# Kernel optimization log

Measured on AMD Instinct MI355X. Metric: run time of the kernel, lower is better.

Reference implementation:

```python
import jax, jax.numpy as jnp
import numpy as np
from jax import lax

B = 8; IMG = 224; P = 16; D = 192; DEPTH = 8
H = IMG // P; W = H; L = H * W
D_IN = 384; D_STATE = 16; D_CONV = 4; DT_R = 12; NCLS = 1000
EPS = 1e-5


def _ln(x, w, b):
    m = x.mean(-1, keepdims=True)
    v = ((x - m) ** 2).mean(-1, keepdims=True)
    return (x - m) * lax.rsqrt(v + EPS) * w + b


def _mixer(seq, p):
    # seq: (B, L, D) -> Mamba selective-scan mixer
    xz = jnp.einsum('bld,ed->ble', seq, p['in_proj_w'])  # (B,L,2*D_IN)
    u, z = jnp.split(xz, 2, axis=-1)
    # causal depthwise conv1d over L
    uc = lax.conv_general_dilated(u.transpose(0, 2, 1), p['conv_w'][:, None, :], (1,),
                                  [(D_CONV - 1, 0)], feature_group_count=D_IN,
                                  dimension_numbers=('NCH', 'OIH', 'NCH'))
    u = jax.nn.silu(uc.transpose(0, 2, 1) + p['conv_b'])
    xdbl = jnp.einsum('bld,ed->ble', u, p['x_proj_w'])  # (B,L,DT_R+2*D_STATE)
    dt = xdbl[..., :DT_R]
    Bm = xdbl[..., DT_R:DT_R + D_STATE]
    Cm = xdbl[..., DT_R + D_STATE:]
    delta = jax.nn.softplus(jnp.einsum('blr,dr->bld', dt, p['dt_w']) + p['dt_b'])
    A = -jnp.exp(p['A_log'])  # (D_IN, D_STATE)

    def step(h, inp):
        d_t, B_t, C_t, u_t = inp  # (b,D_IN),(b,N),(b,N),(b,D_IN)
        h = h * jnp.exp(d_t[..., None] * A) + (d_t * u_t)[..., None] * B_t[:, None, :]
        return h, jnp.einsum('bdn,bn->bd', h, C_t)

    h0 = jnp.zeros((seq.shape[0], D_IN, D_STATE), seq.dtype)
    _, ys = lax.scan(step, h0, (delta.transpose(1, 0, 2), Bm.transpose(1, 0, 2),
                                Cm.transpose(1, 0, 2), u.transpose(1, 0, 2)))
    y = ys.transpose(1, 0, 2) + u * p['D']
    y = y * jax.nn.silu(z)
    return jnp.einsum('bld,cd->blc', y, p['out_proj_w'])


def _stack(seq, params):
    # Block: residual = residual + hidden; hidden = mixer(LN(residual))
    def body(carry, p):
        hidden, residual = carry
        residual = residual + hidden
        hidden = _mixer(_ln(residual, p['ln_w'], p['ln_b']), p)
        return (hidden, residual), None

    (hidden, residual), _ = lax.scan(body, (seq, jnp.zeros_like(seq)), params)
    return hidden + residual


def _forward(x, patch_w, patch_b, pe_ln_w, pe_ln_b, ln_w, ln_b, in_proj_w, conv_w,
             conv_b, x_proj_w, dt_w, dt_b, A_log, Dp, out_proj_w, out_norm_w,
             out_norm_b, head_ln_w, head_ln_b, head_w, head_b):
    b = x.shape[0]
    # patch embed: conv(stride=patch) + LayerNorm over channels
    feat = lax.conv_general_dilated(x, patch_w, (P, P), 'VALID',
                                    dimension_numbers=('NCHW', 'OIHW', 'NCHW'))
    feat = feat + patch_b[None, :, None, None]  # (B, D, H, W)
    feat = _ln(feat.transpose(0, 2, 3, 1), pe_ln_w, pe_ln_b).transpose(0, 3, 1, 2)
    # CrossScan: 4 directional unrollings
    x0 = feat.reshape(b, D, L)
    x1 = feat.transpose(0, 1, 3, 2).reshape(b, D, L)
    xs = jnp.stack([x0, x1, x0[..., ::-1], x1[..., ::-1]], axis=1)  # (B,4,D,L)
    dirs = xs.transpose(1, 0, 3, 2)  # (4,B,L,D)
    params = {'ln_w': ln_w, 'ln_b': ln_b, 'in_proj_w': in_proj_w, 'conv_w': conv_w,
              'conv_b': conv_b, 'x_proj_w': x_proj_w, 'dt_w': dt_w, 'dt_b': dt_b,
              'A_log': A_log, 'D': Dp, 'out_proj_w': out_proj_w}
    outs = jax.vmap(_stack)(dirs, params)  # (4,B,L,D)
    # CrossMerge
    ys = outs.transpose(1, 0, 3, 2)  # (B,4,D,L)
    ym = ys[:, 0:2] + ys[:, 2:4][..., ::-1]
    y = ym[:, 0] + ym[:, 1].reshape(b, D, W, H).transpose(0, 1, 3, 2).reshape(b, D, L)
    y = _ln(y.transpose(0, 2, 1), out_norm_w, out_norm_b)  # (B,L,D)
    y = _ln(y.reshape(b, H, W, D), head_ln_w, head_ln_b)
    return y.mean(axis=(1, 2)) @ head_w.T + head_b  # (B, NCLS)


def setup_inputs() -> dict:
    key = jax.random.key(0)
    ks = jax.random.split(key, 10)
    rn = lambda k, s, sc=0.02: jax.random.normal(k, s, jnp.float32) * sc
    A_init = jnp.broadcast_to(jnp.arange(1, D_STATE + 1, dtype=jnp.float32),
                              (4, DEPTH, D_IN, D_STATE))
    return {
        'x': jax.random.normal(ks[0], (B, 3, IMG, IMG), jnp.float32),
        'patch_w': rn(ks[1], (D, 3, P, P)),
        'patch_b': jnp.zeros((D,), jnp.float32),
        'pe_ln_w': jnp.ones((D,), jnp.float32),
        'pe_ln_b': jnp.zeros((D,), jnp.float32),
        'ln_w': jnp.ones((4, DEPTH, D), jnp.float32),
        'ln_b': jnp.zeros((4, DEPTH, D), jnp.float32),
        'in_proj_w': rn(ks[2], (4, DEPTH, 2 * D_IN, D)),
        'conv_w': rn(ks[3], (4, DEPTH, D_IN, D_CONV), 0.1),
        'conv_b': jnp.zeros((4, DEPTH, D_IN), jnp.float32),
        'x_proj_w': rn(ks[4], (4, DEPTH, DT_R + 2 * D_STATE, D_IN)),
        'dt_w': rn(ks[5], (4, DEPTH, D_IN, DT_R), 0.1),
        'dt_b': jnp.log(jnp.expm1(0.01)) + rn(ks[6], (4, DEPTH, D_IN), 0.02),
        'A_log': jnp.log(A_init),
        'Dp': jnp.ones((4, DEPTH, D_IN), jnp.float32),
        'out_proj_w': rn(ks[7], (4, DEPTH, D, D_IN)),
        'out_norm_w': jnp.ones((D,), jnp.float32),
        'out_norm_b': jnp.zeros((D,), jnp.float32),
        'head_ln_w': jnp.ones((D,), jnp.float32),
        'head_ln_b': jnp.zeros((D,), jnp.float32),
        'head_w': rn(ks[8], (NCLS, D)),
        'head_b': jnp.zeros((NCLS,), jnp.float32),
    }


def reference(x, patch_w, patch_b, pe_ln_w, pe_ln_b, ln_w, ln_b, in_proj_w, conv_w,
              conv_b, x_proj_w, dt_w, dt_b, A_log, Dp, out_proj_w, out_norm_w,
              out_norm_b, head_ln_w, head_ln_b, head_w, head_b):
    return _forward(x, patch_w, patch_b, pe_ln_w, pe_ln_b, ln_w, ln_b, in_proj_w,
                    conv_w, conv_b, x_proj_w, dt_w, dt_b, A_log, Dp, out_proj_w,
                    out_norm_w, out_norm_b, head_ln_w, head_ln_b, head_w, head_b)
```

## Files before the change

### kernel.cpp

```cpp
#include <hip/hip_runtime.h>

#define B_ 8
#define IMGSZ 224
#define PATCH 16
#define D_ 192
#define DEPTH_ 8
#define H_ 14
#define W_ 14
#define L_ 196
#define DIN 384
#define DSTATE 16
#define DCONV 4
#define DTR 12
#define NCLS_ 1000
#define EPS_ 1e-5f
#define ROWS_PER_DIR (B_*L_)
#define M_TOTAL (4*ROWS_PER_DIR)

typedef unsigned short ushort_t;
typedef unsigned int uint_t;
typedef __attribute__((ext_vector_type(8)))  short bf16x8;
typedef __attribute__((ext_vector_type(16))) float f32x16;

__device__ __forceinline__ ushort_t f2bf(float f) {
  uint_t u = __builtin_bit_cast(uint_t, f);
  u += 0x7fffu + ((u >> 16) & 1u);
  return (ushort_t)(u >> 16);
}

__global__ __launch_bounds__(256) void k_cvt3(
    const float* __restrict__ s0, const float* __restrict__ s1,
    const float* __restrict__ s2, ushort_t* __restrict__ dst)
{
  int i = blockIdx.x*256 + threadIdx.x;
  if (i >= 1806336) return;
  const float* src;
  int off;
  if (i < 36864)        { src = s0; off = i; }
  else if (i < 1216512) { src = s1; off = i - 36864; }
  else                  { src = s2; off = i - 1216512; }
  float4 v = reinterpret_cast<const float4*>(src)[off];
  ushort4 o;
  o.x = f2bf(v.x); o.y = f2bf(v.y); o.z = f2bf(v.z); o.w = f2bf(v.w);
  reinterpret_cast<ushort4*>(dst)[i] = o;
}

__global__ __launch_bounds__(256) void k_cvt_xw(const float* __restrict__ src,
                                                ushort_t* __restrict__ dst)
{
  int idx = blockIdx.x*256 + threadIdx.x;
  if (idx >= 32*64*384) return;
  int g = idx / (64*384);
  int r = (idx / 384) % 64;
  int k = idx % 384;
  float v = (r < 44) ? src[((size_t)g*44 + r)*384 + k] : 0.f;
  dst[idx] = f2bf(v);
}

__global__ __launch_bounds__(256) void k_im2col(const float* __restrict__ x,
                                                ushort_t* __restrict__ Xp)
{
  int idx = blockIdx.x*256 + threadIdx.x;
  if (idx >= ROWS_PER_DIR*768) return;
  int row = idx / 768, k = idx - row*768;
  int b = row / L_, l = row - b*L_;
  int hh = l / W_, ww = l - hh*W_;
  int c = k >> 8, rem = k & 255, pi = rem >> 4, pj = rem & 15;
  float v = x[(((size_t)b*3 + c)*IMGSZ + hh*PATCH + pi)*IMGSZ + ww*PATCH + pj];
  Xp[idx] = f2bf(v);
}

template<int KT>
__global__ __launch_bounds__(64) void k_gemm2(
    const ushort_t* __restrict__ X, const ushort_t* __restrict__ W,
    float* __restrict__ C, int N, int nb, int wstride, int rows_per_dir)
{
  int row0 = blockIdx.x*32, col0 = blockIdx.y*64;
  int dir = row0 / rows_per_dir;
  const ushort_t* Wp = W + (size_t)dir*wstride;
  int l = threadIdx.x;
  int r31 = l & 31, khalf = (l >> 5)*8;
  const ushort_t* aptr  = X  + (size_t)(row0 + r31)*KT + khalf;
  const ushort_t* b0ptr = Wp + (size_t)(col0 + r31)*KT + khalf;
  const ushort_t* b1ptr = b0ptr + (size_t)32*KT;
  f32x16 acc00 = {}, acc01 = {}, acc10 = {}, acc11 = {};
  #pragma unroll
  for (int k = 0; k < KT; k += 32) {
    bf16x8 a0 = *reinterpret_cast<const bf16x8*>(aptr + k);
    bf16x8 a1 = *reinterpret_cast<const bf16x8*>(aptr + k + 16);
    bf16x8 b00 = *reinterpret_cast<const bf16x8*>(b0ptr + k);
    bf16x8 b01 = *reinterpret_cast<const bf16x8*>(b0ptr + k + 16);
    bf16x8 b10 = *reinterpret_cast<const bf16x8*>(b1ptr + k);
    bf16x8 b11 = *reinterpret_cast<const bf16x8*>(b1ptr + k + 16);
    acc00 = __builtin_amdgcn_mfma_f32_32x32x16_bf16(a0, b00, acc00, 0, 0, 0);
    acc01 = __builtin_amdgcn_mfma_f32_32x32x16_bf16(a1, b01, acc01, 0, 0, 0);
    acc10 = __builtin_amdgcn_mfma_f32_32x32x16_bf16(a0, b10, acc10, 0, 0, 0);
    acc11 = __builtin_amdgcn_mfma_f32_32x32x16_bf16(a1, b11, acc11, 0, 0, 0);
  }
  int c0 = col0 + r31, c1 = col0 + 32 + r31;
  #pragma unroll
  for (int r = 0; r < 16; ++r) {
    int row = (r & 3) + 8*(r >> 2) + 4*(l >> 5);
    float* crow = C + (size_t)(row0 + row)*N;
    if (c0 < nb) crow[c0] = acc00[r] + acc01[r];
    if (c1 < nb) crow[c1] = acc10[r] + acc11[r];
  }
}

__global__ __launch_bounds__(64) void k_peln(
    const float* __restrict__ Cp, const float* __restrict__ pb,
    const float* __restrict__ plw, const float* __restrict__ plb,
    const float* __restrict__ lnw, const float* __restrict__ lnb,
    float* __restrict__ residual, ushort_t* __restrict__ xln)
{
  int blk = blockIdx.x;
  int b = blk / L_, l = blk - b*L_;
  int hh = l / W_, ww = l - hh*W_;
  int lane = threadIdx.x;
  float v[3]; float s = 0.f;
  #pragma unroll
  for (int i = 0; i < 3; ++i) {
    int d = lane + i*64;
    float t = Cp[(size_t)blk*D_ + d] + pb[d];
    v[i] = t; s += t;
  }
  #pragma unroll
  for (int off = 32; off; off >>= 1) s += __shfl_xor(s, off);
  float m = s*(1.f/D_); float q = 0.f;
  #pragma unroll
  for (int i = 0; i < 3; ++i) { float dd = v[i]-m; q += dd*dd; }
  #pragma unroll
  for (int off = 32; off; off >>= 1) q += __shfl_xor(q, off);
  float inv = rsqrtf(q*(1.f/D_)+EPS_);
  float nv[3]; s = 0.f;
  #pragma unroll
  for (int i = 0; i < 3; ++i) {
    int d = lane + i*64;
    nv[i] = (v[i]-m)*inv*plw[d] + plb[d];
    s += nv[i];
  }
  #pragma unroll
  for (int off = 32; off; off >>= 1) s += __shfl_xor(s, off);
  float m2 = s*(1.f/D_); q = 0.f;
  #pragma unroll
  for (int i = 0; i < 3; ++i) { float dd = nv[i]-m2; q += dd*dd; }
  #pragma unroll
  for (int off = 32; off; off >>= 1) q += __shfl_xor(q, off);
  float inv2 = rsqrtf(q*(1.f/D_)+EPS_);
  int l1 = ww*W_ + hh;
  size_t rr[4];
  rr[0] = ((size_t)(0*B_+b))*L_ + l;
  rr[1] = ((size_t)(1*B_+b))*L_ + l1;
  rr[2] = ((size_t)(2*B_+b))*L_ + (L_-1-l);
  rr[3] = ((size_t)(3*B_+b))*L_ + (L_-1-l1);
  #pragma unroll
  for (int i = 0; i < 3; ++i) {
    int d = lane + i*64;
    float nrm = (nv[i]-m2)*inv2;
    #pragma unroll
    for (int k = 0; k < 4; ++k) {
      residual[rr[k]*D_+d] = nv[i];
      xln[rr[k]*D_+d] = f2bf(nrm*lnw[(size_t)(k*DEPTH_)*D_+d] + lnb[(size_t)(k*DEPTH_)*D_+d]);
    }
  }
}

__global__ __launch_bounds__(256) void k_conv(
    const float* __restrict__ xz, const float* __restrict__ cw, const float* __restrict__ cb,
    float* __restrict__ u, ushort_t* __restrict__ ub, int layer)
{
  int idx = blockIdx.x*256 + threadIdx.x;
  if (idx >= M_TOTAL*96) return;
  int row = idx / 96, d4 = (idx - row*96)*4;
  int kdir = row / ROWS_PER_DIR;
  int l = row % L_;
  size_t pbase = (size_t)(kdir*DEPTH_+layer)*DIN + d4;
  const float* cwp = cw + pbase*DCONV;
  float wv[16];
  #pragma unroll
  for (int i = 0; i < 4; ++i)
    ((float4*)wv)[i] = ((const float4*)cwp)[i];
  float4 bias = *reinterpret_cast<const float4*>(&cb[pbase]);
  float acc[4] = {bias.x, bias.y, bias.z, bias.w};
  #pragma unroll
  for (int t = 0; t < DCONV; ++t) {
    int ll = l - 3 + t;
    if (ll >= 0) {
      float4 xv = *reinterpret_cast<const float4*>(&xz[((size_t)row + (ll - l))*768 + d4]);
      acc[0] += xv.x * wv[0*4 + t];
      acc[1] += xv.y * wv[1*4 + t];
      acc[2] += xv.z * wv[2*4 + t];
      acc[3] += xv.w * wv[3*4 + t];
    }
  }
  float4 o; ushort4 ob;
  o.x = acc[0] / (1.f + __expf(-acc[0]));
  o.y = acc[1] / (1.f + __expf(-acc[1]));
  o.z = acc[2] / (1.f + __expf(-acc[2]));
  o.w = acc[3] / (1.f + __expf(-acc[3]));
  ob.x = f2bf(o.x); ob.y = f2bf(o.y); ob.z = f2bf(o.z); ob.w = f2bf(o.w);
  *reinterpret_cast<float4*>(&u[(size_t)row*DIN + d4]) = o;
  *reinterpret_cast<ushort4*>(&ub[(size_t)row*DIN + d4]) = ob;
}

#define SCHUNK 14
#define NCHUNK 14
__global__ __launch_bounds__(256, 3) void k_scan(
    const float* __restrict__ u, const float* __restrict__ xdbl,
    const float* __restrict__ xz,
    const float* __restrict__ Alog, const float* __restrict__ Dp,
    const float* __restrict__ dtw, const float* __restrict__ dtb,
    ushort_t* __restrict__ yg, int layer)
{
  int blk = blockIdx.x;
  int kdir = blk / (B_*24);
  int rem = blk % (B_*24);
  int b = rem / 24, dc = rem % 24;
  int tid = threadIdx.x;
  int st = tid & 15, ch = tid >> 4;
  size_t pl = (size_t)(kdir*DEPTH_+layer)*DIN + dc*16 + ch;
  float a = -expf(Alog[pl*DSTATE + st]);
  size_t rowbase = ((size_t)kdir*B_ + b)*L_;

  int ll = tid >> 4, cc = tid & 15;
  bool ldr = tid < 224;
  size_t plc = (size_t)(kdir*DEPTH_+layer)*DIN + dc*16 + cc;
  float Dv3 = Dp[plc];
  float dwt[12]; float dbias = dtb[plc];
  #pragma unroll
  for (int i = 0; i < 3; ++i)
    ((float4*)dwt)[i] = ((const float4*)(dtw + plc*DTR))[i];

  __shared__ __align__(16) float sd[16][20], su[16][20], sB[16][20],
                                 sC[16][20], sz[16][20];
  __shared__ __align__(16) float sp[SCHUNK][16][20];

  float rd=0.f, ru=0.f, rB=0.f, rC=0.f, rz=0.f;
  if (ldr) {
    size_t r = rowbase + ll;
    float xv[12];
    #pragma unroll
    for (int i = 0; i < 3; ++i) ((float4*)xv)[i] = ((const float4*)(xdbl + r*44))[i];
    float acc = dbias;
    #pragma unroll
    for (int t = 0; t < DTR; ++t) acc += xv[t]*dwt[t];
    rd = (acc > 20.f) ? acc : log1pf(__expf(acc));
    ru = u[r*DIN + dc*16 + cc];
    rB = xdbl[r*44 + DTR + cc];
    rC = xdbl[r*44 + DTR + DSTATE + cc];
    rz = xz[r*768 + DIN + dc*16 + cc];
  }

  float h = 0.f;
  for (int chk = 0; chk < NCHUNK; ++chk) {
    if (ldr) { sd[cc][ll]=rd; su[cc][ll]=ru; sB[cc][ll]=rB; sC[cc][ll]=rC; sz[cc][ll]=rz; }
    __syncthreads();
    if (chk+1 < NCHUNK && ldr) {
      size_t r = rowbase + (chk+1)*SCHUNK + ll;
      float xv[12];
      #pragma unroll
      for (int i = 0; i < 3; ++i) ((float4*)xv)[i] = ((const float4*)(xdbl + r*44))[i];
      float acc = dbias;
      #pragma unroll
      for (int t = 0; t < DTR; ++t) acc += xv[t]*dwt[t];
      rd = (acc > 20.f) ? acc : log1pf(__expf(acc));
      ru = u[r*DIN + dc*16 + cc];
      rB = xdbl[r*44 + DTR + cc];
      rC = xdbl[r*44 + DTR + DSTATE + cc];
      rz = xz[r*768 + DIN + dc*16 + cc];
    }
    float dlv[16], ulv[16], Bvv[16], Cvv[16];
    #pragma unroll
    for (int i = 0; i < 4; ++i) {
      ((float4*)dlv)[i] = ((const float4*)&sd[ch][0])[i];
      ((float4*)ulv)[i] = ((const float4*)&su[ch][0])[i];
      ((float4*)Bvv)[i] = ((const float4*)&sB[st][0])[i];
      ((float4*)Cvv)[i] = ((const float4*)&sC[st][0])[i];
    }
    float E[SCHUNK];
    #pragma unroll
    for (int l = 0; l < SCHUNK; ++l) E[l] = __expf(dlv[l]*a);
    #pragma unroll
    for (int l = 0; l < SCHUNK; ++l) {
      h = h*E[l] + dlv[l]*ulv[l]*Bvv[l];
      sp[l][ch][st] = h*Cvv[l];
    }
    __syncthreads();
    if (ldr) {
      float pv[16];
      #pragma unroll
      for (int i = 0; i < 4; ++i)
        ((float4*)pv)[i] = ((const float4*)&sp[ll][cc][0])[i];
      float s = 0.f;
      #pragma unroll
      for (int i = 0; i < 16; ++i) s += pv[i];
      float ul = su[cc][ll];
      float z  = sz[cc][ll];
      float yv = (s + ul*Dv3) * (z / (1.f + __expf(-z)));
      yg[(rowbase + chk*SCHUNK + ll)*DIN + dc*16 + cc] = f2bf(yv);
    }
    __syncthreads();
  }
}

template<int LAST>
__global__ __launch_bounds__(384) void k_outln(
    const ushort_t* __restrict__ X, const ushort_t* __restrict__ W,
    float* __restrict__ residual,
    const float* __restrict__ lnw, const float* __restrict__ lnb,
    ushort_t* __restrict__ xln, int layer)
{
  int row0 = blockIdx.x*32;
  int dir = row0 / ROWS_PER_DIR;
  const ushort_t* Wp = W + (size_t)dir*(DEPTH_*D_*DIN);
  int tid = threadIdx.x;
  int wv = tid >> 6;
  int l  = tid & 63;
  int col0 = wv*32;
  int r31 = l & 31, khalf = (l >> 5)*8;
  const ushort_t* aptr = X  + (size_t)(row0 + r31)*DIN + khalf;
  const ushort_t* bptr = Wp + (size_t)(col0 + r31)*DIN + khalf;
  f32x16 acc0 = {}, acc1 = {};
  #pragma unroll
  for (int k = 0; k < DIN; k += 32) {
    bf16x8 a0 = *reinterpret_cast<const bf16x8*>(aptr + k);
    bf16x8 b0 = *reinterpret_cast<const bf16x8*>(bptr + k);
    bf16x8 a1 = *reinterpret_cast<const bf16x8*>(aptr + k + 16);
    bf16x8 b1 = *reinterpret_cast<const bf16x8*>(bptr + k + 16);
    acc0 = __builtin_amdgcn_mfma_f32_32x32x16_bf16(a0, b0, acc0, 0, 0, 0);
    acc1 = __builtin_amdgcn_mfma_f32_32x32x16_bf16(a1, b1, acc1, 0, 0, 0);
  }
  __shared__ __align__(16) float Cs[32][196];
  __shared__ float sred[32][12], qred[32][12], sm[32], si[32];
  #pragma unroll
  for (int r = 0; r < 16; ++r) {
    int row = (r & 3) + 8*(r >> 2) + 4*(l >> 5);
    Cs[row][col0 + r31] = acc0[r] + acc1[r];
  }
  __syncthreads();
  int rr = tid / 12, jj = tid - rr*12;
  int c0 = jj*16;
  float* resrow = residual + (size_t)(row0+rr)*D_ + c0;
  float v[16];
  float s = 0.f, q = 0.f;
  #pragma unroll
  for (int i = 0; i < 16; i += 4) {
    float4 rv = *reinterpret_cast<const float4*>(resrow + i);
    float4 cv = *reinterpret_cast<const float4*>(&Cs[rr][c0 + i]);
    v[i+0] = rv.x + cv.x; v[i+1] = rv.y + cv.y;
    v[i+2] = rv.z + cv.z; v[i+3] = rv.w + cv.w;
  }
  #pragma unroll
  for (int i = 0; i < 16; ++i) { s += v[i]; q += v[i]*v[i]; }
  #pragma unroll
  for (int i = 0; i < 16; i += 4) {
    float4 o = make_float4(v[i], v[i+1], v[i+2], v[i+3]);
    *reinterpret_cast<float4*>(resrow + i) = o;
  }
  if (!LAST) {
    sred[rr][jj] = s; qred[rr][jj] = q;
    __syncthreads();
    if (tid < 32) {
      float S = 0.f, Q = 0.f;
      #pragma unroll
      for (int j = 0; j < 12; ++j) { S += sred[tid][j]; Q += qred[tid][j]; }
      float m = S*(1.f/D_);
      float var = Q*(1.f/D_) - m*m;
      sm[tid] = m; si[tid] = rsqrtf(var + EPS_);
    }
    __syncthreads();
    float m = sm[rr], inv = si[rr];
    const float* w = lnw + (size_t)(dir*DEPTH_ + layer + 1)*D_ + c0;
    const float* bb = lnb + (size_t)(dir*DEPTH_ + layer + 1)*D_ + c0;
    ushort_t* xrow = xln + (size_t)(row0+rr)*D_ + c0;
    #pragma unroll
    for (int i = 0; i < 16; ++i)
      xrow[i] = f2bf((v[i]-m)*inv*w[i] + bb[i]);
  }
}

__global__ __launch_bounds__(64) void k_combine(
    const float* __restrict__ res,
    const float* __restrict__ onw, const float* __restrict__ onb,
    const float* __restrict__ hlw, const float* __restrict__ hlb,
    float* __restrict__ ynorm)
{
  int blk = blockIdx.x;
  int b = blk / L_, l = blk % L_;
  int hh = l / W_, ww = l % W_;
  int l1 = ww*W_ + hh;
  size_t r0 = ((size_t)(0*B_+b))*L_ + l;
  size_t r1 = ((size_t)(1*B_+b))*L_ + l1;
  size_t r2 = ((size_t)(2*B_+b))*L_ + (L_-1-l);
  size_t r3 = ((size_t)(3*B_+b))*L_ + (L_-1-l1);
  int lane = threadIdx.x;
  float v[3]; float s = 0.f;
  #pragma unroll
  for (int i=0;i<3;i++){
    int d = lane + i*64;
    float t = res[r0*D_+d] + res[r1*D_+d] + res[r2*D_+d] + res[r3*D_+d];
    v[i]=t; s+=t;
  }
  #pragma unroll
  for (int off=32;off;off>>=1) s += __shfl_xor(s,off);
  float m = s*(1.f/D_); float q=0.f;
  #pragma unroll
  for (int i=0;i<3;i++){ float dd=v[i]-m; q+=dd*dd; }
  #pragma unroll
  for (int off=32;off;off>>=1) q += __shfl_xor(q,off);
  float inv = rsqrtf(q*(1.f/D_)+EPS_);
  float v2[3]; s = 0.f;
  #pragma unroll
  for (int i=0;i<3;i++){ int d=lane+i*64; float t=(v[i]-m)*inv*onw[d]+onb[d]; v2[i]=t; s+=t; }
  #pragma unroll
  for (int off=32;off;off>>=1) s += __shfl_xor(s,off);
  float m2 = s*(1.f/D_); q=0.f;
  #pragma unroll
  for (int i=0;i<3;i++){ float dd=v2[i]-m2; q+=dd*dd; }
  #pragma unroll
  for (int off=32;off;off>>=1) q += __shfl_xor(q,off);
  float inv2 = rsqrtf(q*(1.f/D_)+EPS_);
  #pragma unroll
  for (int i=0;i<3;i++){ int d=lane+i*64; ynorm[((size_t)b*L_+l)*D_+d] = (v2[i]-m2)*inv2*hlw[d]+hlb[d]; }
}

__global__ __launch_bounds__(192) void k_mean(const float* __restrict__ ynorm, float* __restrict__ ybar)
{
  int b = blockIdx.x, d = threadIdx.x;
  float s = 0.f;
  for (int l = 0; l < L_; ++l) s += ynorm[((size_t)b*L_+l)*D_ + d];
  ybar[b*D_+d] = s * (1.f/L_);
}

__global__ __launch_bounds__(256) void k_head(
    const float* __restrict__ ybar, const float* __restrict__ hw, const float* __restrict__ hb,
    float* __restrict__ out)
{
  __shared__ float ys[D_];
  int b = blockIdx.x >> 2;
  int c = (blockIdx.x & 3)*256 + threadIdx.x;
  for (int i = threadIdx.x; i < D_; i += 256) ys[i] = ybar[b*D_+i];
  __syncthreads();
  if (c < NCLS_) {
    float acc = hb[c];
    const float* wr = hw + (size_t)c*D_;
    for (int dd = 0; dd < D_; dd += 4) {
      float4 a4 = *reinterpret_cast<const float4*>(&ys[dd]);
      float4 b4 = *reinterpret_cast<const float4*>(&wr[dd]);
      acc += a4.x*b4.x + a4.y*b4.y + a4.z*b4.z + a4.w*b4.w;
    }
    out[(size_t)b*NCLS_ + c] = acc;
  }
}

extern "C" void kernel_launch(void* const* d_in, const int* in_sizes, int n_in,
                              void* d_out, int out_size, void* d_ws, size_t ws_size,
                              hipStream_t stream)
{
  const float* x          = (const float*)d_in[0];
  const float* patch_w    = (const float*)d_in[1];
  const float* patch_b    = (const float*)d_in[2];
  const float* pe_ln_w    = (const float*)d_in[3];
  const float* pe_ln_b    = (const float*)d_in[4];
  const float* ln_w       = (const float*)d_in[5];
  const float* ln_b       = (const float*)d_in[6];
  const float* in_proj_w  = (const float*)d_in[7];
  const float* conv_w     = (const float*)d_in[8];
  const float* conv_b     = (const float*)d_in[9];
  const float* x_proj_w   = (const float*)d_in[10];
  const float* dt_w       = (const float*)d_in[11];
  const float* dt_b       = (const float*)d_in[12];
  const float* A_log      = (const float*)d_in[13];
  const float* Dp         = (const float*)d_in[14];
  const float* out_proj_w = (const float*)d_in[15];
  const float* out_norm_w = (const float*)d_in[16];
  const float* out_norm_b = (const float*)d_in[17];
  const float* head_ln_w  = (const float*)d_in[18];
  const float* head_ln_b  = (const float*)d_in[19];
  const float* head_w     = (const float*)d_in[20];
  const float* head_b     = (const float*)d_in[21];
  float* out = (float*)d_out;

  float* ws = (float*)d_ws;
  float*   residual = ws;
  float*   xz       = residual + 1204224;
  float*   u        = xz + 4816896;
  float*   xdbl     = u + 2408448;
  ushort_t* u_bf    = (ushort_t*)(xdbl + 275968);
  ushort_t* yg_bf   = u_bf + 2408448;
  ushort_t* xln_bf  = yg_bf + 2408448;
  ushort_t* wbf     = xln_bf + 1204224;
  ushort_t* pw_bf   = wbf;
  ushort_t* inw_bf  = wbf + 147456;
  ushort_t* outw_bf = inw_bf + 4718592;
  ushort_t* xw_bf   = outw_bf + 2359296;
  ushort_t* Xp      = (ushort_t*)xz;
  float*   C_patch  = xz + 602112;
  float*   ynorm    = u;
  float*   ybar     = u + 301056;

  k_cvt3<<<(1806336+255)/256, 256, 0, stream>>>(patch_w, in_proj_w, out_proj_w, wbf);
  k_cvt_xw<<<(32*64*384+255)/256, 256, 0, stream>>>(x_proj_w, xw_bf);

  k_im2col<<<(ROWS_PER_DIR*768+255)/256, 256, 0, stream>>>(x, Xp);
  k_gemm2<768><<<dim3(ROWS_PER_DIR/32, 3), 64, 0, stream>>>(
      Xp, pw_bf, C_patch, D_, D_, 0, ROWS_PER_DIR);
  k_peln<<<ROWS_PER_DIR, 64, 0, stream>>>(C_patch, patch_b, pe_ln_w, pe_ln_b,
                                          ln_w, ln_b, residual, xln_bf);

  for (int layer = 0; layer < DEPTH_; ++layer) {
    k_gemm2<192><<<dim3(M_TOTAL/32, 12), 64, 0, stream>>>(
        xln_bf, inw_bf + (size_t)layer*768*D_, xz, 768, 768, DEPTH_*768*D_, ROWS_PER_DIR);
    k_conv<<<(M_TOTAL*96+255)/256, 256, 0, stream>>>(xz, conv_w, conv_b, u, u_bf, layer);
    k_gemm2<384><<<dim3(M_TOTAL/32, 1), 64, 0, stream>>>(
        u_bf, xw_bf + (size_t)layer*64*384, xdbl, 44, 44, DEPTH_*64*384, ROWS_PER_DIR);
    k_scan<<<4*B_*24, 256, 0, stream>>>(u, xdbl, xz, A_log, Dp, dt_w, dt_b, yg_bf, layer);
    if (layer < DEPTH_-1)
      k_outln<0><<<M_TOTAL/32, 384, 0, stream>>>(
          yg_bf, outw_bf, residual, ln_w, ln_b, xln_bf, layer);
    else
      k_outln<1><<<M_TOTAL/32, 384, 0, stream>>>(
          yg_bf, outw_bf, residual, ln_w, ln_b, xln_bf, layer);
  }

  k_combine<<<B_*L_, 64, 0, stream>>>(residual, out_norm_w, out_norm_b,
                                      head_ln_w, head_ln_b, ynorm);
  k_mean<<<B_, 192, 0, stream>>>(ynorm, ybar);
  k_head<<<B_*4, 256, 0, stream>>>(ybar, head_w, head_b, out);
}
```

Before: 677.6 us.

## Store in_proj output as bf16 and fuse causal conv into x_proj GEMM and scan

The in_proj GEMM now writes xz in bf16 instead of fp32, halving that intermediate's memory traffic. The separate conv kernel and its u/u_bf buffers are removed. The conv plus SiLU is recomputed on the fly inside a new x_proj GEMM kernel to build its A operand, and again inside the scan to produce u. This saves a kernel launch and a large write/read round trip, at the cost of duplicated conv arithmetic and extra bf16 rounding of z and the conv inputs.

```diff
diff --git a/kernel.cpp b/kernel.cpp
--- a/kernel.cpp
+++ b/kernel.cpp
@@ -27,6 +27,10 @@
   u += 0x7fffu + ((u >> 16) & 1u);
   return (ushort_t)(u >> 16);
 }
+__device__ __forceinline__ float bf2f(ushort_t s) {
+  uint_t u = ((uint_t)s) << 16;
+  return __builtin_bit_cast(float, u);
+}
 
 __global__ __launch_bounds__(256) void k_cvt3(
     const float* __restrict__ s0, const float* __restrict__ s1,
@@ -70,10 +74,10 @@
   Xp[idx] = f2bf(v);
 }
 
-template<int KT>
+template<int KT, int OBF>
 __global__ __launch_bounds__(64) void k_gemm2(
     const ushort_t* __restrict__ X, const ushort_t* __restrict__ W,
-    float* __restrict__ C, int N, int nb, int wstride, int rows_per_dir)
+    void* __restrict__ C, int N, int nb, int wstride, int rows_per_dir)
 {
   int row0 = blockIdx.x*32, col0 = blockIdx.y*64;
   int dir = row0 / rows_per_dir;
@@ -101,9 +105,18 @@
   #pragma unroll
   for (int r = 0; r < 16; ++r) {
     int row = (r & 3) + 8*(r >> 2) + 4*(l >> 5);
-    float* crow = C + (size_t)(row0 + row)*N;
-    if (c0 < nb) crow[c0] = acc00[r] + acc01[r];
-    if (c1 < nb) crow[c1] = acc10[r] + acc11[r];
+    size_t base = (size_t)(row0 + row)*N;
+    float v0 = acc00[r] + acc01[r];
+    float v1 = acc10[r] + acc11[r];
+    if (OBF) {
+      ushort_t* crow = (ushort_t*)C + base;
+      if (c0 < nb) crow[c0] = f2bf(v0);
+      if (c1 < nb) crow[c1] = f2bf(v1);
+    } else {
+      float* crow = (float*)C + base;
+      if (c0 < nb) crow[c0] = v0;
+      if (c1 < nb) crow[c1] = v1;
+    }
   }
 }
 
@@ -165,51 +178,87 @@
   }
 }
 
-__global__ __launch_bounds__(256) void k_conv(
-    const float* __restrict__ xz, const float* __restrict__ cw, const float* __restrict__ cb,
-    float* __restrict__ u, ushort_t* __restrict__ ub, int layer)
-{
-  int idx = blockIdx.x*256 + threadIdx.x;
-  if (idx >= M_TOTAL*96) return;
-  int row = idx / 96, d4 = (idx - row*96)*4;
-  int kdir = row / ROWS_PER_DIR;
+__device__ __forceinline__ bf16x8 conv8(
+    const ushort_t* __restrict__ xzb, int row, int l, int ch0,
+    const float* __restrict__ scw, const float* __restrict__ scb)
+{
+  float acc[8];
+  #pragma unroll
+  for (int j = 0; j < 8; ++j) acc[j] = scb[ch0+j];
+  #pragma unroll
+  for (int t = 0; t < 4; ++t) {
+    int lt = l - 3 + t;
+    if (lt >= 0) {
+      bf16x8 xv = *reinterpret_cast<const bf16x8*>(xzb + (size_t)(row-3+t)*768 + ch0);
+      #pragma unroll
+      for (int j = 0; j < 8; ++j)
+        acc[j] += bf2f((ushort_t)xv[j]) * scw[(ch0+j)*4 + t];
+    }
+  }
+  bf16x8 o;
+  #pragma unroll
+  for (int j = 0; j < 8; ++j) {
+    float uv = acc[j] / (1.f + __expf(-acc[j]));
+    o[j] = (short)f2bf(uv);
+  }
+  return o;
+}
+
+__global__ __launch_bounds__(64) void k_xprojc(
+    const ushort_t* __restrict__ xzb,
+    const float* __restrict__ cw, const float* __restrict__ cb,
+    const ushort_t* __restrict__ xw, float* __restrict__ xdbl, int layer)
+{
+  int row0 = blockIdx.x*32;
+  int dir = row0 / ROWS_PER_DIR;
+  __shared__ __align__(16) float scw[DIN*DCONV];
+  __shared__ float scb[DIN];
+  int tid = threadIdx.x;
+  {
+    const float* cwp = cw + (size_t)(dir*DEPTH_+layer)*DIN*DCONV;
+    const float* cbp = cb + (size_t)(dir*DEPTH_+layer)*DIN;
+    for (int i = tid; i < 384; i += 64) {
+      reinterpret_cast<float4*>(scw)[i] = reinterpret_cast<const float4*>(cwp)[i];
+      scb[i] = cbp[i];
+    }
+  }
+  __syncthreads();
+  int r31 = tid & 31, khalf = (tid >> 5)*8;
+  int row = row0 + r31;
   int l = row % L_;
-  size_t pbase = (size_t)(kdir*DEPTH_+layer)*DIN + d4;
-  const float* cwp = cw + pbase*DCONV;
-  float wv[16];
-  #pragma unroll
-  for (int i = 0; i < 4; ++i)
-    ((float4*)wv)[i] = ((const float4*)cwp)[i];
-  float4 bias = *reinterpret_cast<const float4*>(&cb[pbase]);
-  float acc[4] = {bias.x, bias.y, bias.z, bias.w};
-  #pragma unroll
-  for (int t = 0; t < DCONV; ++t) {
-    int ll = l - 3 + t;
-    if (ll >= 0) {
-      float4 xv = *reinterpret_cast<const float4*>(&xz[((size_t)row + (ll - l))*768 + d4]);
-      acc[0] += xv.x * wv[0*4 + t];
-      acc[1] += xv.y * wv[1*4 + t];
-      acc[2] += xv.z * wv[2*4 + t];
-      acc[3] += xv.w * wv[3*4 + t];
-    }
-  }
-  float4 o; ushort4 ob;
-  o.x = acc[0] / (1.f + __expf(-acc[0]));
-  o.y = acc[1] / (1.f + __expf(-acc[1]));
-  o.z = acc[2] / (1.f + __expf(-acc[2]));
-  o.w = acc[3] / (1.f + __expf(-acc[3]));
-  ob.x = f2bf(o.x); ob.y = f2bf(o.y); ob.z = f2bf(o.z); ob.w = f2bf(o.w);
-  *reinterpret_cast<float4*>(&u[(size_t)row*DIN + d4]) = o;
-  *reinterpret_cast<ushort4*>(&ub[(size_t)row*DIN + d4]) = ob;
+  const ushort_t* b0ptr = xw + (size_t)(dir*DEPTH_+layer)*64*384 + (size_t)r31*384 + khalf;
+  const ushort_t* b1ptr = b0ptr + (size_t)32*384;
+  f32x16 acc00 = {}, acc01 = {}, acc10 = {}, acc11 = {};
+  #pragma unroll 4
+  for (int k = 0; k < DIN; k += 32) {
+    bf16x8 a0 = conv8(xzb, row, l, k + khalf, scw, scb);
+    bf16x8 a1 = conv8(xzb, row, l, k + khalf + 16, scw, scb);
+    bf16x8 b00 = *reinterpret_cast<const bf16x8*>(b0ptr + k);
+    bf16x8 b01 = *reinterpret_cast<const bf16x8*>(b0ptr + k + 16);
+    bf16x8 b10 = *reinterpret_cast<const bf16x8*>(b1ptr + k);
+    bf16x8 b11 = *reinterpret_cast<const bf16x8*>(b1ptr + k + 16);
+    acc00 = __builtin_amdgcn_mfma_f32_32x32x16_bf16(a0, b00, acc00, 0, 0, 0);
+    acc01 = __builtin_amdgcn_mfma_f32_32x32x16_bf16(a1, b01, acc01, 0, 0, 0);
+    acc10 = __builtin_amdgcn_mfma_f32_32x32x16_bf16(a0, b10, acc10, 0, 0, 0);
+    acc11 = __builtin_amdgcn_mfma_f32_32x32x16_bf16(a1, b11, acc11, 0, 0, 0);
+  }
+  int c0 = r31, c1 = 32 + r31;
+  #pragma unroll
+  for (int r = 0; r < 16; ++r) {
+    int rr = (r & 3) + 8*(r >> 2) + 4*(tid >> 5);
+    float* crow = xdbl + (size_t)(row0 + rr)*44;
+    crow[c0] = acc00[r] + acc01[r];
+    if (c1 < 44) crow[c1] = acc10[r] + acc11[r];
+  }
 }
 
 #define SCHUNK 14
 #define NCHUNK 14
 __global__ __launch_bounds__(256, 3) void k_scan(
-    const float* __restrict__ u, const float* __restrict__ xdbl,
-    const float* __restrict__ xz,
+    const ushort_t* __restrict__ xzb, const float* __restrict__ xdbl,
     const float* __restrict__ Alog, const float* __restrict__ Dp,
     const float* __restrict__ dtw, const float* __restrict__ dtb,
+    const float* __restrict__ cw, const float* __restrict__ cb,
     ushort_t* __restrict__ yg, int layer)
 {
   int blk = blockIdx.x;
@@ -230,6 +279,8 @@
   #pragma unroll
   for (int i = 0; i < 3; ++i)
     ((float4*)dwt)[i] = ((const float4*)(dtw + plc*DTR))[i];
+  float cwv[4]; float cbv = cb[plc];
+  *((float4*)cwv) = *((const float4*)(cw + plc*DCONV));
 
   __shared__ __align__(16) float sd[16][20], su[16][20], sB[16][20],
                                  sC[16][20], sz[16][20];
@@ -237,18 +288,25 @@
 
   float rd=0.f, ru=0.f, rB=0.f, rC=0.f, rz=0.f;
   if (ldr) {
-    size_t r = rowbase + ll;
+    int l0 = ll;
+    int row = (int)(rowbase + l0);
     float xv[12];
     #pragma unroll
-    for (int i = 0; i < 3; ++i) ((float4*)xv)[i] = ((const float4*)(xdbl + r*44))[i];
+    for (int i = 0; i < 3; ++i) ((float4*)xv)[i] = ((const float4*)(xdbl + (size_t)row*44))[i];
     float acc = dbias;
     #pragma unroll
     for (int t = 0; t < DTR; ++t) acc += xv[t]*dwt[t];
     rd = (acc > 20.f) ? acc : log1pf(__expf(acc));
-    ru = u[r*DIN + dc*16 + cc];
-    rB = xdbl[r*44 + DTR + cc];
-    rC = xdbl[r*44 + DTR + DSTATE + cc];
-    rz = xz[r*768 + DIN + dc*16 + cc];
+    float ua = cbv;
+    #pragma unroll
+    for (int t = 0; t < 4; ++t) {
+      int lt = l0 - 3 + t;
+      if (lt >= 0) ua += bf2f(xzb[(size_t)(row-3+t)*768 + dc*16 + cc]) * cwv[t];
+    }
+    ru = ua / (1.f + __expf(-ua));
+    rB = xdbl[(size_t)row*44 + DTR + cc];
+    rC = xdbl[(size_t)row*44 + DTR + DSTATE + cc];
+    rz = bf2f(xzb[(size_t)row*768 + DIN + dc*16 + cc]);
   }
 
   float h = 0.f;
@@ -256,18 +314,25 @@
     if (ldr) { sd[cc][ll]=rd; su[cc][ll]=ru; sB[cc][ll]=rB; sC[cc][ll]=rC; sz[cc][ll]=rz; }
     __syncthreads();
     if (chk+1 < NCHUNK && ldr) {
-      size_t r = rowbase + (chk+1)*SCHUNK + ll;
+      int l0 = (chk+1)*SCHUNK + ll;
+      int row = (int)(rowbase + l0);
       float xv[12];
       #pragma unroll
-      for (int i = 0; i < 3; ++i) ((float4*)xv)[i] = ((const float4*)(xdbl + r*44))[i];
+      for (int i = 0; i < 3; ++i) ((float4*)xv)[i] = ((const float4*)(xdbl + (size_t)row*44))[i];
       float acc = dbias;
       #pragma unroll
       for (int t = 0; t < DTR; ++t) acc += xv[t]*dwt[t];
       rd = (acc > 20.f) ? acc : log1pf(__expf(acc));
-      ru = u[r*DIN + dc*16 + cc];
-      rB = xdbl[r*44 + DTR + cc];
-      rC = xdbl[r*44 + DTR + DSTATE + cc];
-      rz = xz[r*768 + DIN + dc*16 + cc];
+      float ua = cbv;
+      #pragma unroll
+      for (int t = 0; t < 4; ++t) {
+        int lt = l0 - 3 + t;
+        if (lt >= 0) ua += bf2f(xzb[(size_t)(row-3+t)*768 + dc*16 + cc]) * cwv[t];
+      }
+      ru = ua / (1.f + __expf(-ua));
+      rB = xdbl[(size_t)row*44 + DTR + cc];
+      rC = xdbl[(size_t)row*44 + DTR + DSTATE + cc];
+      rz = bf2f(xzb[(size_t)row*768 + DIN + dc*16 + cc]);
     }
     float dlv[16], ulv[16], Bvv[16], Cvv[16];
     #pragma unroll
@@ -482,39 +547,37 @@
   float* out = (float*)d_out;
 
   float* ws = (float*)d_ws;
-  float*   residual = ws;
-  float*   xz       = residual + 1204224;
-  float*   u        = xz + 4816896;
-  float*   xdbl     = u + 2408448;
-  ushort_t* u_bf    = (ushort_t*)(xdbl + 275968);
-  ushort_t* yg_bf   = u_bf + 2408448;
-  ushort_t* xln_bf  = yg_bf + 2408448;
-  ushort_t* wbf     = xln_bf + 1204224;
-  ushort_t* pw_bf   = wbf;
-  ushort_t* inw_bf  = wbf + 147456;
-  ushort_t* outw_bf = inw_bf + 4718592;
-  ushort_t* xw_bf   = outw_bf + 2359296;
-  ushort_t* Xp      = (ushort_t*)xz;
-  float*   C_patch  = xz + 602112;
-  float*   ynorm    = u;
-  float*   ybar     = u + 301056;
+  float*    residual = ws;
+  ushort_t* xz_bf    = (ushort_t*)(residual + 1204224);
+  float*    xdbl     = (float*)(xz_bf + 4816896);
+  ushort_t* yg_bf    = (ushort_t*)(xdbl + 275968);
+  ushort_t* xln_bf   = yg_bf + 2408448;
+  ushort_t* wbf      = xln_bf + 1204224;
+  ushort_t* pw_bf    = wbf;
+  ushort_t* inw_bf   = wbf + 147456;
+  ushort_t* outw_bf  = inw_bf + 4718592;
+  ushort_t* xw_bf    = outw_bf + 2359296;
+  ushort_t* Xp       = xz_bf;
+  float*    C_patch  = (float*)(xz_bf + 1204224);
+  float*    ynorm    = (float*)yg_bf;
+  float*    ybar     = ynorm + 301056;
 
   k_cvt3<<<(1806336+255)/256, 256, 0, stream>>>(patch_w, in_proj_w, out_proj_w, wbf);
   k_cvt_xw<<<(32*64*384+255)/256, 256, 0, stream>>>(x_proj_w, xw_bf);
 
   k_im2col<<<(ROWS_PER_DIR*768+255)/256, 256, 0, stream>>>(x, Xp);
-  k_gemm2<768><<<dim3(ROWS_PER_DIR/32, 3), 64, 0, stream>>>(
+  k_gemm2<768,0><<<dim3(ROWS_PER_DIR/32, 3), 64, 0, stream>>>(
       Xp, pw_bf, C_patch, D_, D_, 0, ROWS_PER_DIR);
   k_peln<<<ROWS_PER_DIR, 64, 0, stream>>>(C_patch, patch_b, pe_ln_w, pe_ln_b,
                                           ln_w, ln_b, residual, xln_bf);
 
   for (int layer = 0; layer < DEPTH_; ++layer) {
-    k_gemm2<192><<<dim3(M_TOTAL/32, 12), 64, 0, stream>>>(
-        xln_bf, inw_bf + (size_t)layer*768*D_, xz, 768, 768, DEPTH_*768*D_, ROWS_PER_DIR);
-    k_conv<<<(M_TOTAL*96+255)/256, 256, 0, stream>>>(xz, conv_w, conv_b, u, u_bf, layer);
-    k_gemm2<384><<<dim3(M_TOTAL/32, 1), 64, 0, stream>>>(
-        u_bf, xw_bf + (size_t)layer*64*384, xdbl, 44, 44, DEPTH_*64*384, ROWS_PER_DIR);
-    k_scan<<<4*B_*24, 256, 0, stream>>>(u, xdbl, xz, A_log, Dp, dt_w, dt_b, yg_bf, layer);
+    k_gemm2<192,1><<<dim3(M_TOTAL/32, 12), 64, 0, stream>>>(
+        xln_bf, inw_bf + (size_t)layer*768*D_, xz_bf, 768, 768, DEPTH_*768*D_, ROWS_PER_DIR);
+    k_xprojc<<<M_TOTAL/32, 64, 0, stream>>>(
+        xz_bf, conv_w, conv_b, xw_bf, xdbl, layer);
+    k_scan<<<4*B_*24, 256, 0, stream>>>(
+        xz_bf, xdbl, A_log, Dp, dt_w, dt_b, conv_w, conv_b, yg_bf, layer);
     if (layer < DEPTH_-1)
       k_outln<0><<<M_TOTAL/32, 384, 0, stream>>>(
           yg_bf, outw_bf, residual, ln_w, ln_b, xln_bf, layer);
```

Result: slower. 783.2 us (+15.6%).
